# Performance work log

Hardware: AMD Instinct MI355X
Metric: run time of the kernel (lower is better)

## Reference

```python
import jax, jax.numpy as jnp
import numpy as np

NUM_FEATURES = 1_000_000
EMB_DIM = 16
NUM_FIELDS = 39
CIN_SIZES = (200, 200, 200)
DNN_SIZES = (400, 400)


def setup_inputs() -> dict:
    key = jax.random.key(0)
    ks = jax.random.split(key, 16)
    B = 2048
    inp = {}
    inp["feature_ids"] = jax.random.randint(ks[0], (B, NUM_FIELDS), 0, NUM_FEATURES)
    inp["feature_vals"] = jax.random.uniform(ks[1], (B, NUM_FIELDS), dtype=jnp.float32)
    # embeddings (xavier-normal-ish scale)
    inp["emb"] = jax.random.normal(ks[2], (NUM_FEATURES, EMB_DIM), jnp.float32) * 0.02
    inp["bias_emb"] = jax.random.normal(ks[3], (NUM_FEATURES, 1), jnp.float32) * 0.02
    # CIN conv1d (kernel size 1) weights: (out, in)
    field_nums = [NUM_FIELDS]
    for i, size in enumerate(CIN_SIZES):
        cin_in = field_nums[-1] * NUM_FIELDS
        inp[f"cin_W{i}"] = jax.random.normal(ks[4 + i], (size, cin_in), jnp.float32) / np.sqrt(cin_in)
        inp[f"cin_b{i}"] = jnp.zeros((size,), jnp.float32)
        field_nums.append(size // 2 if i != len(CIN_SIZES) - 1 else size)
    # DNN linears: (out, in)
    last = NUM_FIELDS * EMB_DIM
    for i, size in enumerate(DNN_SIZES):
        inp[f"dnn_W{i}"] = jax.random.normal(ks[8 + i], (size, last), jnp.float32) / np.sqrt(last)
        inp[f"dnn_b{i}"] = jnp.zeros((size,), jnp.float32)
        last = size
    hidden_size = sum(CIN_SIZES[:-1]) // 2 + CIN_SIZES[-1]  # 400
    fc_in = hidden_size + DNN_SIZES[-1]
    inp["fc_W"] = jax.random.normal(ks[12], (1, fc_in), jnp.float32) / np.sqrt(fc_in)
    inp["fc_b"] = jnp.zeros((1,), jnp.float32)
    return inp


def _forward(feature_ids, feature_vals, emb, bias_emb,
             cin_W0, cin_b0, cin_W1, cin_b1, cin_W2, cin_b2,
             dnn_W0, dnn_b0, dnn_W1, dnn_b1, fc_W, fc_b):
    B = feature_ids.shape[0]
    inputs = emb[feature_ids] * feature_vals[:, :, None]        # [B, F, D]
    input_biases = bias_emb[feature_ids][..., 0] * feature_vals  # [B, F]

    # CIN
    Ws = (cin_W0, cin_W1, cin_W2)
    bs = (cin_b0, cin_b1, cin_b2)
    h = inputs
    finals = []
    n_layers = len(CIN_SIZES)
    for i in range(n_layers):
        size = CIN_SIZES[i]
        x = jnp.einsum('bhd,bmd->bhmd', h, inputs)              # [B, H, F, D]
        x = x.reshape(B, -1, EMB_DIM)                           # [B, H*F, D]
        x = jnp.einsum('bcd,oc->bod', x, Ws[i]) + bs[i][None, :, None]  # 1x1 conv
        x = jax.nn.relu(x)
        if i != n_layers - 1:
            h, direct = x[:, : size // 2], x[:, size // 2:]
        else:
            direct = x
        finals.append(direct)
    cin_result = jnp.sum(jnp.concatenate(finals, axis=1), axis=-1)  # [B, hidden]

    # DNN
    d = inputs.reshape(B, -1)
    d = jax.nn.relu(d @ dnn_W0.T + dnn_b0)
    d = jax.nn.relu(d @ dnn_W1.T + dnn_b1)

    out = (jnp.concatenate((cin_result, d), axis=1) @ fc_W.T + fc_b)[:, 0]
    return out + jnp.sum(input_biases, axis=1)                  # [B]


def reference(feature_ids, feature_vals, emb, bias_emb,
              cin_W0, cin_b0, cin_W1, cin_b1, cin_W2, cin_b2,
              dnn_W0, dnn_b0, dnn_W1, dnn_b1, fc_W, fc_b):
    return _forward(feature_ids, feature_vals, emb, bias_emb,
                    cin_W0, cin_b0, cin_W1, cin_b1, cin_W2, cin_b2,
                    dnn_W0, dnn_b0, dnn_W1, dnn_b1, fc_W, fc_b)
```

## Files before the change

kernel.cpp:

```cpp
#include <hip/hip_runtime.h>

#define B 2048
#define NF 39
#define D 16

typedef __bf16 bf16x8 __attribute__((ext_vector_type(8)));
typedef float f32x4 __attribute__((ext_vector_type(4)));

__device__ __forceinline__ void lds_barrier() {
  asm volatile("s_waitcnt lgkmcnt(0)" ::: "memory");
  __builtin_amdgcn_s_barrier();
}

__global__ __launch_bounds__(256) void gather_kernel(
    const int* __restrict__ fid, const float* __restrict__ fval,
    const float* __restrict__ emb, const float* __restrict__ bias_emb,
    float* __restrict__ inputs, float* __restrict__ biassum) {
  int b = blockIdx.x;
  __shared__ int ids[NF];
  __shared__ float vals[NF];
  int t = threadIdx.x;
  if (t < NF) { ids[t] = fid[b * NF + t]; vals[t] = fval[b * NF + t]; }
  __syncthreads();
  for (int i = t; i < NF * D; i += 256) {
    int f = i >> 4, d = i & 15;
    inputs[b * NF * D + i] = emb[(long)ids[f] * D + d] * vals[f];
  }
  if (t < 64) {
    float pb = (t < NF) ? bias_emb[ids[t]] * vals[t] : 0.f;
#pragma unroll
    for (int m = 32; m >= 1; m >>= 1) pb += __shfl_xor(pb, m);
    if (t == 0) biassum[b] = pb;
  }
}

__device__ __forceinline__ void prep_cin_one(const float* __restrict__ W,
                                             __bf16* __restrict__ Wg,
                                             int Hreal, int idx) {
  int l = idx & 63;
  int mt = (idx >> 6) % 13;
  int c = idx / (13 * 64);
  int o = mt * 16 + (l & 15);
  int kb = c * 32 + ((l >> 4) << 3);
  int rowlen = Hreal * 39;
  bf16x8 v;
#pragma unroll
  for (int j = 0; j < 8; ++j) {
    int k = kb + j;
    int h = k / 40;
    int m = k - h * 40;
    float val = 0.f;
    if (o < 200 && h < Hreal && m < 39) val = W[(long)o * rowlen + h * 39 + m];
    v[j] = (__bf16)val;
  }
  *reinterpret_cast<bf16x8*>(Wg + (long)idx * 8) = v;
}

__device__ __forceinline__ void prep_dnn_one(const float* __restrict__ W,
                                             __bf16* __restrict__ Wd,
                                             int IN, int idx) {
  int l = idx & 63;
  int tt = (idx >> 6) % 25;
  int c = idx / (25 * 64);
  int o = tt * 16 + (l & 15);
  int kb = c * 32 + ((l >> 4) << 3);
  bf16x8 v;
#pragma unroll
  for (int j = 0; j < 8; ++j) {
    int k = kb + j;
    v[j] = (k < IN) ? (__bf16)W[(long)o * IN + k] : (__bf16)0.f;
  }
  *reinterpret_cast<bf16x8*>(Wd + (long)idx * 8) = v;
}

#define PREP_T0 (50 * 13 * 64)
#define PREP_T12 (126 * 13 * 64)
#define PREP_T3 (20 * 25 * 64)
#define PREP_T4 (13 * 25 * 64)
#define PREP_TOTAL (PREP_T0 + 2 * PREP_T12 + PREP_T3 + PREP_T4)

__global__ void prep_all(const float* __restrict__ cW0, const float* __restrict__ cW1,
                         const float* __restrict__ cW2, const float* __restrict__ dW0,
                         const float* __restrict__ dW1, __bf16* __restrict__ Wg0,
                         __bf16* __restrict__ Wg1, __bf16* __restrict__ Wg2,
                         __bf16* __restrict__ Wd0, __bf16* __restrict__ Wd1) {
  int idx = blockIdx.x * 256 + threadIdx.x;
  if (idx < PREP_T0) { prep_cin_one(cW0, Wg0, 39, idx); return; }
  idx -= PREP_T0;
  if (idx < PREP_T12) { prep_cin_one(cW1, Wg1, 100, idx); return; }
  idx -= PREP_T12;
  if (idx < PREP_T12) { prep_cin_one(cW2, Wg2, 100, idx); return; }
  idx -= PREP_T12;
  if (idx < PREP_T3) { prep_dnn_one(dW0, Wd0, 624, idx); return; }
  idx -= PREP_T3;
  if (idx < PREP_T4) prep_dnn_one(dW1, Wd1, 400, idx);
}

__device__ __forceinline__ void form_x2(const float* Hs, const float* Zs,
                                        __bf16* xbuf, int k0, int col) {
  int h = (int)((unsigned)k0 / 40u);
  int m0 = k0 - h * 40;
  float hv = Hs[h * 32 + col];
  const float4* zp = reinterpret_cast<const float4*>(Zs + col * 44 + m0);
  float4 za = zp[0], zb = zp[1];
  bf16x8 xv;
  xv[0] = (__bf16)(hv * za.x); xv[1] = (__bf16)(hv * za.y);
  xv[2] = (__bf16)(hv * za.z); xv[3] = (__bf16)(hv * za.w);
  xv[4] = (__bf16)(hv * zb.x); xv[5] = (__bf16)(hv * zb.y);
  xv[6] = (__bf16)(hv * zb.z); xv[7] = (__bf16)(hv * zb.w);
  int g = (k0 >> 3) & 7;
  *reinterpret_cast<bf16x8*>(
      reinterpret_cast<char*>(xbuf) + col * 128 + ((g * 16) ^ ((col & 7) << 4))) = xv;
}

template <int PLO, int NP, int NST, int SPLIT>
__device__ __forceinline__ void cin_layer2(
    float* Hs, const float* Zs, __bf16* Xs,
    const __bf16* __restrict__ Wg, const float* __restrict__ bias,
    float* __restrict__ cin_out, int col_offset, int bbase, int t) {
  constexpr int TLO = PLO >> 1;
  constexpr int THI = (PLO + NP - 1) >> 1;
  constexpr int TN = THI - TLO + 1;
  const int l = t & 63;
  const int q = l >> 4, dd = l & 15;
  const int xcol = t & 31;
  const int xg = (t >> 5) & 7;
  const __bf16* wl = Wg + l * 8;

  f32x4 acc[NP] = {};
  bf16x8 wf[TN][2], wfn[TN][2];
#pragma unroll
  for (int i = 0; i < TN; ++i)
#pragma unroll
    for (int c2 = 0; c2 < 2; ++c2)
      wf[i][c2] = *reinterpret_cast<const bf16x8*>(
          wl + (long)((c2 * 13 + TLO + i) * 64) * 8);

  form_x2(Hs, Zs, Xs, xg * 8, xcol);
  lds_barrier();

  for (int s = 0; s < NST; ++s) {
    __bf16* xcur = Xs + (s & 1) * 2048;
    __bf16* xnxt = Xs + ((s + 1) & 1) * 2048;
    const bool more = (s + 1 < NST);
    if (more) {
#pragma unroll
      for (int i = 0; i < TN; ++i)
#pragma unroll
        for (int c2 = 0; c2 < 2; ++c2)
          wfn[i][c2] = *reinterpret_cast<const bf16x8*>(
              wl + (long)((((s + 1) * 2 + c2) * 13 + TLO + i) * 64) * 8);
    }
    bf16x8 bfr[2][2];
#pragma unroll
    for (int f = 0; f < 2; ++f)
#pragma unroll
      for (int c2 = 0; c2 < 2; ++c2) {
        int col = f * 16 + dd;
        int g = c2 * 4 + q;
        bfr[f][c2] = *reinterpret_cast<const bf16x8*>(
            reinterpret_cast<const char*>(xcur) + col * 128 +
            ((g * 16) ^ ((col & 7) << 4)));
      }
    if (more) form_x2(Hs, Zs, xnxt, (s + 1) * 64 + xg * 8, xcol);
    __builtin_amdgcn_s_setprio(1);
#pragma unroll
    for (int i = 0; i < NP; ++i) {
      const int p = PLO + i;
      const int ti = (p >> 1) - TLO;
      const int f = p & 1;
      acc[i] = __builtin_amdgcn_mfma_f32_16x16x32_bf16(wf[ti][0], bfr[f][0],
                                                       acc[i], 0, 0, 0);
      acc[i] = __builtin_amdgcn_mfma_f32_16x16x32_bf16(wf[ti][1], bfr[f][1],
                                                       acc[i], 0, 0, 0);
    }
    __builtin_amdgcn_s_setprio(0);
    lds_barrier();
    if (more) {
#pragma unroll
      for (int i = 0; i < TN; ++i) {
        wf[i][0] = wfn[i][0];
        wf[i][1] = wfn[i][1];
      }
    }
  }

#pragma unroll
  for (int i = 0; i < NP; ++i) {
    const int p = PLO + i;
    const int tt = p >> 1, f = p & 1;
    const int b = bbase + f;
#pragma unroll
    for (int r = 0; r < 4; ++r) {
      int o = tt * 16 + q * 4 + r;
      if (o < 200) {
        float x = fmaxf(acc[i][r] + bias[o], 0.f);
        if (SPLIT && o < 100) {
          Hs[o * 32 + f * 16 + dd] = x;
        } else {
          x += __shfl_xor(x, 1);
          x += __shfl_xor(x, 2);
          x += __shfl_xor(x, 4);
          x += __shfl_xor(x, 8);
          if (dd == 0) cin_out[b * 400 + col_offset + o - (SPLIT ? 100 : 0)] = x;
        }
      }
    }
  }
  lds_barrier();
}

template <int PLO, int NP>
__device__ __forceinline__ void cin_all2(
    float* Hs, const float* Zs, __bf16* Xs, const __bf16* Wg0,
    const __bf16* Wg1, const __bf16* Wg2, const float* cb0, const float* cb1,
    const float* cb2, float* cinres, int bbase, int t) {
  cin_layer2<PLO, NP, 25, 1>(Hs, Zs, Xs, Wg0, cb0, cinres, 0, bbase, t);
  cin_layer2<PLO, NP, 63, 1>(Hs, Zs, Xs, Wg1, cb1, cinres, 100, bbase, t);
  cin_layer2<PLO, NP, 63, 0>(Hs, Zs, Xs, Wg2, cb2, cinres, 200, bbase, t);
}

__global__ __launch_bounds__(256, 4) void cin_fused2(
    const float* __restrict__ Zin, const __bf16* __restrict__ Wg0,
    const __bf16* __restrict__ Wg1, const __bf16* __restrict__ Wg2,
    const float* __restrict__ cb0, const float* __restrict__ cb1,
    const float* __restrict__ cb2, float* __restrict__ cinres) {
  __shared__ float Hs[101 * 32];
  __shared__ float Zs[32 * 44];
  __shared__ __bf16 Xs[2 * 2048];
  const int t = threadIdx.x;
  const int bbase = blockIdx.x * 2;

  for (int i = t; i < 32 * 44; i += 256) {
    int col = i / 44, m = i - (i / 44) * 44;
    int b = bbase + (col >> 4), d = col & 15;
    Zs[i] = (m < NF) ? Zin[((long)b * NF + m) * 16 + d] : 0.f;
  }
  for (int i = t; i < 41 * 32; i += 256) {
    int h = i >> 5, col = i & 31;
    int b = bbase + (col >> 4), d = col & 15;
    Hs[i] = (h < NF) ? Zin[((long)b * NF + h) * 16 + d] : 0.f;
  }
  if (t < 32) Hs[100 * 32 + t] = 0.f;
  __syncthreads();

  const int w = t >> 6;
  switch (w) {
    case 0: cin_all2<0, 7>(Hs, Zs, Xs, Wg0, Wg1, Wg2, cb0, cb1, cb2, cinres, bbase, t); break;
    case 1: cin_all2<7, 7>(Hs, Zs, Xs, Wg0, Wg1, Wg2, cb0, cb1, cb2, cinres, bbase, t); break;
    case 2: cin_all2<14, 6>(Hs, Zs, Xs, Wg0, Wg1, Wg2, cb0, cb1, cb2, cinres, bbase, t); break;
    default: cin_all2<20, 6>(Hs, Zs, Xs, Wg0, Wg1, Wg2, cb0, cb1, cb2, cinres, bbase, t); break;
  }
}

template <int IN>
__device__ __forceinline__ void dnn_stage_load(const float* __restrict__ x,
                                               int bg, int c, int t,
                                               float4& a, float4& b2) {
  int b = t >> 2, kb = t & 3;
  int k0 = c * 32 + kb * 8;
  if (k0 < IN) {
    const float4* p =
        reinterpret_cast<const float4*>(x + (long)(bg * 64 + b) * IN + k0);
    a = p[0];
    b2 = p[1];
  } else {
    a = make_float4(0.f, 0.f, 0.f, 0.f);
    b2 = make_float4(0.f, 0.f, 0.f, 0.f);
  }
}

__device__ __forceinline__ void dnn_stage_write(__bf16* Xs, int t, float4 a,
                                                float4 b2) {
  int b = t >> 2, kb = t & 3;
  bf16x8 v;
  v[0] = (__bf16)a.x;  v[1] = (__bf16)a.y;  v[2] = (__bf16)a.z;  v[3] = (__bf16)a.w;
  v[4] = (__bf16)b2.x; v[5] = (__bf16)b2.y; v[6] = (__bf16)b2.z; v[7] = (__bf16)b2.w;
  *reinterpret_cast<bf16x8*>(Xs + ((kb * 64 + b) << 3)) = v;
}

template <int IN, int NCH>
__global__ __launch_bounds__(256) void dnn_mfma2(
    const float* __restrict__ x, const __bf16* __restrict__ Wd,
    const float* __restrict__ bias, float* __restrict__ out) {
  __shared__ __bf16 Xs[2 * 2048];
  const int bg = blockIdx.x / 25;
  const int tile = blockIdx.x - bg * 25;
  const int t = threadIdx.x;
  const int w = t >> 6, l = t & 63;
  const int q = l >> 4, dd = l & 15;
  const __bf16* wl = Wd + l * 8;

  f32x4 acc = {};
  bf16x8 wf = *reinterpret_cast<const bf16x8*>(wl + (long)(tile * 64) * 8);

  float4 ra, rb;
  dnn_stage_load<IN>(x, bg, 0, t, ra, rb);
  dnn_stage_write(Xs, t, ra, rb);
  lds_barrier();

  for (int c = 0; c < NCH; ++c) {
    __bf16* cur = Xs + (c & 1) * 2048;
    __bf16* nxt = Xs + ((c + 1) & 1) * 2048;
    const bool more = (c + 1 < NCH);
    bf16x8 wfn;
    if (more) {
      dnn_stage_load<IN>(x, bg, c + 1, t, ra, rb);
      wfn = *reinterpret_cast<const bf16x8*>(
          wl + (long)(((c + 1) * 25 + tile) * 64) * 8);
    }
    bf16x8 bfr = *reinterpret_cast<const bf16x8*>(cur + ((q * 64 + w * 16 + dd) << 3));
    acc = __builtin_amdgcn_mfma_f32_16x16x32_bf16(wf, bfr, acc, 0, 0, 0);
    if (more) dnn_stage_write(nxt, t, ra, rb);
    lds_barrier();
    if (more) wf = wfn;
  }

  const int b = bg * 64 + w * 16 + dd;
#pragma unroll
  for (int r = 0; r < 4; ++r) {
    int o = tile * 16 + q * 4 + r;
    out[(long)b * 400 + o] = fmaxf(acc[r] + bias[o], 0.f);
  }
}

__global__ __launch_bounds__(256) void final_kernel(
    const float* __restrict__ cin, const float* __restrict__ d1,
    const float* __restrict__ fcW, const float* __restrict__ fcb,
    const float* __restrict__ biassum, float* __restrict__ out) {
  int b = blockIdx.x, t = threadIdx.x;
  float p = 0.f;
  for (int i = t; i < 800; i += 256) {
    float v = (i < 400) ? cin[b * 400 + i] : d1[b * 400 + (i - 400)];
    p += v * fcW[i];
  }
#pragma unroll
  for (int m = 32; m >= 1; m >>= 1) p += __shfl_xor(p, m);
  __shared__ float red[4];
  if ((t & 63) == 0) red[t >> 6] = p;
  __syncthreads();
  if (t == 0) out[b] = red[0] + red[1] + red[2] + red[3] + fcb[0] + biassum[b];
}

extern "C" void kernel_launch(void* const* d_in, const int* in_sizes, int n_in,
                              void* d_out, int out_size, void* d_ws,
                              size_t ws_size, hipStream_t stream) {
  (void)in_sizes; (void)n_in; (void)out_size; (void)ws_size;
  const int* fid = (const int*)d_in[0];
  const float* fval = (const float*)d_in[1];
  const float* emb = (const float*)d_in[2];
  const float* bias_emb = (const float*)d_in[3];
  const float* cW0 = (const float*)d_in[4];
  const float* cb0 = (const float*)d_in[5];
  const float* cW1 = (const float*)d_in[6];
  const float* cb1 = (const float*)d_in[7];
  const float* cW2 = (const float*)d_in[8];
  const float* cb2 = (const float*)d_in[9];
  const float* dW0 = (const float*)d_in[10];
  const float* db0 = (const float*)d_in[11];
  const float* dW1 = (const float*)d_in[12];
  const float* db1 = (const float*)d_in[13];
  const float* fcW = (const float*)d_in[14];
  const float* fcb = (const float*)d_in[15];
  float* out = (float*)d_out;

  float* ws = (float*)d_ws;
  float* inputs = ws;  ws += B * NF * D;
  float* biassum = ws; ws += B;
  float* cinres = ws;  ws += B * 400;
  float* dd0 = ws;     ws += B * 400;
  float* dd1 = ws;     ws += B * 400;
  __bf16* Wg0 = (__bf16*)ws; ws += (50 * 13 * 64 * 8) / 2;
  __bf16* Wg1 = (__bf16*)ws; ws += (126 * 13 * 64 * 8) / 2;
  __bf16* Wg2 = (__bf16*)ws; ws += (126 * 13 * 64 * 8) / 2;
  __bf16* Wd0 = (__bf16*)ws; ws += (20 * 25 * 64 * 8) / 2;
  __bf16* Wd1 = (__bf16*)ws; ws += (13 * 25 * 64 * 8) / 2;

  gather_kernel<<<B, 256, 0, stream>>>(fid, fval, emb, bias_emb, inputs, biassum);

  prep_all<<<(PREP_TOTAL + 255) / 256, 256, 0, stream>>>(
      cW0, cW1, cW2, dW0, dW1, Wg0, Wg1, Wg2, Wd0, Wd1);

  cin_fused2<<<B / 2, 256, 0, stream>>>(inputs, Wg0, Wg1, Wg2, cb0, cb1, cb2, cinres);

  dnn_mfma2<624, 20><<<32 * 25, 256, 0, stream>>>(inputs, Wd0, db0, dd0);
  dnn_mfma2<400, 13><<<32 * 25, 256, 0, stream>>>(dd0, Wd1, db1, dd1);

  final_kernel<<<B, 256, 0, stream>>>(cinres, dd1, fcW, fcb, biassum, out);
}
```

Baseline: 234.5 us.

## Process four batch rows per CIN block with 2D wave tiling and ping-pong weight registers

```diff
diff --git a/kernel.cpp b/kernel.cpp
--- a/kernel.cpp
+++ b/kernel.cpp
@@ -96,11 +96,11 @@
   if (idx < PREP_T4) prep_dnn_one(dW1, Wd1, 400, idx);
 }
 
-__device__ __forceinline__ void form_x2(const float* Hs, const float* Zs,
-                                        __bf16* xbuf, int k0, int col) {
+__device__ __forceinline__ void form_x(const float* Hs, const float* Zs,
+                                       __bf16* xbuf, int k0, int col) {
   int h = (int)((unsigned)k0 / 40u);
   int m0 = k0 - h * 40;
-  float hv = Hs[h * 32 + col];
+  float hv = Hs[h * 64 + col];
   const float4* zp = reinterpret_cast<const float4*>(Zs + col * 44 + m0);
   float4 za = zp[0], zb = zp[1];
   bf16x8 xv;
@@ -113,96 +113,98 @@
       reinterpret_cast<char*>(xbuf) + col * 128 + ((g * 16) ^ ((col & 7) << 4))) = xv;
 }
 
-template <int PLO, int NP, int NST, int SPLIT>
-__device__ __forceinline__ void cin_layer2(
+template <int TLO, int TN, int FLO, bool PRE>
+__device__ __forceinline__ void cin_stage(
+    bf16x8 (&wf_use)[TN * 2], bf16x8 (&wf_load)[TN * 2], f32x4 (&acc)[TN * 2],
+    float* Hs, const float* Zs, __bf16* Xs, const __bf16* wl,
+    int s, int q, int dd, int xg, int l) {
+  __bf16* xcur = Xs + (s & 1) * 4096;
+  if (PRE) {
+#pragma unroll
+    for (int i = 0; i < TN; ++i)
+#pragma unroll
+      for (int cc = 0; cc < 2; ++cc)
+        wf_load[i * 2 + cc] = *reinterpret_cast<const bf16x8*>(
+            wl + (long)((((s + 1) * 2 + cc) * 13 + TLO + i) * 64) * 8);
+  }
+  bf16x8 bfr[2][2];
+#pragma unroll
+  for (int f2 = 0; f2 < 2; ++f2)
+#pragma unroll
+    for (int cc = 0; cc < 2; ++cc) {
+      int col = (FLO + f2) * 16 + dd;
+      int g = cc * 4 + q;
+      bfr[f2][cc] = *reinterpret_cast<const bf16x8*>(
+          reinterpret_cast<const char*>(xcur) + col * 128 +
+          ((g * 16) ^ ((col & 7) << 4)));
+    }
+  if (PRE) {
+    __bf16* xnxt = Xs + ((s + 1) & 1) * 4096;
+    form_x(Hs, Zs, xnxt, (s + 1) * 64 + xg * 8, l);
+    form_x(Hs, Zs, xnxt, (s + 1) * 64 + (xg + 4) * 8, l);
+  }
+  __builtin_amdgcn_s_setprio(1);
+#pragma unroll
+  for (int i = 0; i < TN; ++i)
+#pragma unroll
+    for (int f2 = 0; f2 < 2; ++f2)
+#pragma unroll
+      for (int cc = 0; cc < 2; ++cc)
+        acc[i * 2 + f2] = __builtin_amdgcn_mfma_f32_16x16x32_bf16(
+            wf_use[i * 2 + cc], bfr[f2][cc], acc[i * 2 + f2], 0, 0, 0);
+  __builtin_amdgcn_s_setprio(0);
+  lds_barrier();
+}
+
+template <int TLO, int TN, int FLO, int NST, int SPLIT>
+__device__ __forceinline__ void cin_layer3(
     float* Hs, const float* Zs, __bf16* Xs,
     const __bf16* __restrict__ Wg, const float* __restrict__ bias,
     float* __restrict__ cin_out, int col_offset, int bbase, int t) {
-  constexpr int TLO = PLO >> 1;
-  constexpr int THI = (PLO + NP - 1) >> 1;
-  constexpr int TN = THI - TLO + 1;
   const int l = t & 63;
   const int q = l >> 4, dd = l & 15;
-  const int xcol = t & 31;
-  const int xg = (t >> 5) & 7;
+  const int xg = t >> 6;
   const __bf16* wl = Wg + l * 8;
 
-  f32x4 acc[NP] = {};
-  bf16x8 wf[TN][2], wfn[TN][2];
+  f32x4 acc[TN * 2] = {};
+  bf16x8 wfA[TN * 2], wfB[TN * 2];
 #pragma unroll
   for (int i = 0; i < TN; ++i)
 #pragma unroll
-    for (int c2 = 0; c2 < 2; ++c2)
-      wf[i][c2] = *reinterpret_cast<const bf16x8*>(
-          wl + (long)((c2 * 13 + TLO + i) * 64) * 8);
-
-  form_x2(Hs, Zs, Xs, xg * 8, xcol);
+    for (int cc = 0; cc < 2; ++cc)
+      wfA[i * 2 + cc] = *reinterpret_cast<const bf16x8*>(
+          wl + (long)((cc * 13 + TLO + i) * 64) * 8);
+  form_x(Hs, Zs, Xs, xg * 8, l);
+  form_x(Hs, Zs, Xs, (xg + 4) * 8, l);
   lds_barrier();
 
-  for (int s = 0; s < NST; ++s) {
-    __bf16* xcur = Xs + (s & 1) * 2048;
-    __bf16* xnxt = Xs + ((s + 1) & 1) * 2048;
-    const bool more = (s + 1 < NST);
-    if (more) {
-#pragma unroll
-      for (int i = 0; i < TN; ++i)
-#pragma unroll
-        for (int c2 = 0; c2 < 2; ++c2)
-          wfn[i][c2] = *reinterpret_cast<const bf16x8*>(
-              wl + (long)((((s + 1) * 2 + c2) * 13 + TLO + i) * 64) * 8);
-    }
-    bf16x8 bfr[2][2];
-#pragma unroll
-    for (int f = 0; f < 2; ++f)
-#pragma unroll
-      for (int c2 = 0; c2 < 2; ++c2) {
-        int col = f * 16 + dd;
-        int g = c2 * 4 + q;
-        bfr[f][c2] = *reinterpret_cast<const bf16x8*>(
-            reinterpret_cast<const char*>(xcur) + col * 128 +
-            ((g * 16) ^ ((col & 7) << 4)));
-      }
-    if (more) form_x2(Hs, Zs, xnxt, (s + 1) * 64 + xg * 8, xcol);
-    __builtin_amdgcn_s_setprio(1);
-#pragma unroll
-    for (int i = 0; i < NP; ++i) {
-      const int p = PLO + i;
-      const int ti = (p >> 1) - TLO;
-      const int f = p & 1;
-      acc[i] = __builtin_amdgcn_mfma_f32_16x16x32_bf16(wf[ti][0], bfr[f][0],
-                                                       acc[i], 0, 0, 0);
-      acc[i] = __builtin_amdgcn_mfma_f32_16x16x32_bf16(wf[ti][1], bfr[f][1],
-                                                       acc[i], 0, 0, 0);
-    }
-    __builtin_amdgcn_s_setprio(0);
-    lds_barrier();
-    if (more) {
-#pragma unroll
-      for (int i = 0; i < TN; ++i) {
-        wf[i][0] = wfn[i][0];
-        wf[i][1] = wfn[i][1];
-      }
-    }
-  }
-
-#pragma unroll
-  for (int i = 0; i < NP; ++i) {
-    const int p = PLO + i;
-    const int tt = p >> 1, f = p & 1;
-    const int b = bbase + f;
-#pragma unroll
-    for (int r = 0; r < 4; ++r) {
-      int o = tt * 16 + q * 4 + r;
-      if (o < 200) {
-        float x = fmaxf(acc[i][r] + bias[o], 0.f);
-        if (SPLIT && o < 100) {
-          Hs[o * 32 + f * 16 + dd] = x;
-        } else {
-          x += __shfl_xor(x, 1);
-          x += __shfl_xor(x, 2);
-          x += __shfl_xor(x, 4);
-          x += __shfl_xor(x, 8);
-          if (dd == 0) cin_out[b * 400 + col_offset + o - (SPLIT ? 100 : 0)] = x;
+  for (int s2 = 0; s2 < (NST - 1) / 2; ++s2) {
+    cin_stage<TLO, TN, FLO, true>(wfA, wfB, acc, Hs, Zs, Xs, wl, 2 * s2, q, dd, xg, l);
+    cin_stage<TLO, TN, FLO, true>(wfB, wfA, acc, Hs, Zs, Xs, wl, 2 * s2 + 1, q, dd, xg, l);
+  }
+  cin_stage<TLO, TN, FLO, false>(wfA, wfB, acc, Hs, Zs, Xs, wl, NST - 1, q, dd, xg, l);
+
+#pragma unroll
+  for (int i = 0; i < TN; ++i) {
+    const int tt = TLO + i;
+#pragma unroll
+    for (int f2 = 0; f2 < 2; ++f2) {
+      const int f = FLO + f2;
+      const int b = bbase + f;
+#pragma unroll
+      for (int r = 0; r < 4; ++r) {
+        int o = tt * 16 + q * 4 + r;
+        if (o < 200) {
+          float x = fmaxf(acc[i * 2 + f2][r] + bias[o], 0.f);
+          if (SPLIT && o < 100) {
+            Hs[o * 64 + f * 16 + dd] = x;
+          } else {
+            x += __shfl_xor(x, 1);
+            x += __shfl_xor(x, 2);
+            x += __shfl_xor(x, 4);
+            x += __shfl_xor(x, 8);
+            if (dd == 0) cin_out[b * 400 + col_offset + o - (SPLIT ? 100 : 0)] = x;
+          }
         }
       }
     }
@@ -210,46 +212,46 @@
   lds_barrier();
 }
 
-template <int PLO, int NP>
-__device__ __forceinline__ void cin_all2(
+template <int TLO, int TN, int FLO>
+__device__ __forceinline__ void cin_all3(
     float* Hs, const float* Zs, __bf16* Xs, const __bf16* Wg0,
     const __bf16* Wg1, const __bf16* Wg2, const float* cb0, const float* cb1,
     const float* cb2, float* cinres, int bbase, int t) {
-  cin_layer2<PLO, NP, 25, 1>(Hs, Zs, Xs, Wg0, cb0, cinres, 0, bbase, t);
-  cin_layer2<PLO, NP, 63, 1>(Hs, Zs, Xs, Wg1, cb1, cinres, 100, bbase, t);
-  cin_layer2<PLO, NP, 63, 0>(Hs, Zs, Xs, Wg2, cb2, cinres, 200, bbase, t);
-}
-
-__global__ __launch_bounds__(256, 4) void cin_fused2(
+  cin_layer3<TLO, TN, FLO, 25, 1>(Hs, Zs, Xs, Wg0, cb0, cinres, 0, bbase, t);
+  cin_layer3<TLO, TN, FLO, 63, 1>(Hs, Zs, Xs, Wg1, cb1, cinres, 100, bbase, t);
+  cin_layer3<TLO, TN, FLO, 63, 0>(Hs, Zs, Xs, Wg2, cb2, cinres, 200, bbase, t);
+}
+
+__global__ __launch_bounds__(256, 2) void cin_fused3(
     const float* __restrict__ Zin, const __bf16* __restrict__ Wg0,
     const __bf16* __restrict__ Wg1, const __bf16* __restrict__ Wg2,
     const float* __restrict__ cb0, const float* __restrict__ cb1,
     const float* __restrict__ cb2, float* __restrict__ cinres) {
-  __shared__ float Hs[101 * 32];
-  __shared__ float Zs[32 * 44];
-  __shared__ __bf16 Xs[2 * 2048];
+  __shared__ float Hs[101 * 64];
+  __shared__ float Zs[64 * 44];
+  __shared__ __bf16 Xs[2 * 64 * 64];
   const int t = threadIdx.x;
-  const int bbase = blockIdx.x * 2;
-
-  for (int i = t; i < 32 * 44; i += 256) {
+  const int bbase = blockIdx.x * 4;
+
+  for (int i = t; i < 64 * 44; i += 256) {
     int col = i / 44, m = i - (i / 44) * 44;
     int b = bbase + (col >> 4), d = col & 15;
     Zs[i] = (m < NF) ? Zin[((long)b * NF + m) * 16 + d] : 0.f;
   }
-  for (int i = t; i < 41 * 32; i += 256) {
-    int h = i >> 5, col = i & 31;
+  for (int i = t; i < 41 * 64; i += 256) {
+    int h = i >> 6, col = i & 63;
     int b = bbase + (col >> 4), d = col & 15;
     Hs[i] = (h < NF) ? Zin[((long)b * NF + h) * 16 + d] : 0.f;
   }
-  if (t < 32) Hs[100 * 32 + t] = 0.f;
+  if (t < 64) Hs[100 * 64 + t] = 0.f;
   __syncthreads();
 
   const int w = t >> 6;
   switch (w) {
-    case 0: cin_all2<0, 7>(Hs, Zs, Xs, Wg0, Wg1, Wg2, cb0, cb1, cb2, cinres, bbase, t); break;
-    case 1: cin_all2<7, 7>(Hs, Zs, Xs, Wg0, Wg1, Wg2, cb0, cb1, cb2, cinres, bbase, t); break;
-    case 2: cin_all2<14, 6>(Hs, Zs, Xs, Wg0, Wg1, Wg2, cb0, cb1, cb2, cinres, bbase, t); break;
-    default: cin_all2<20, 6>(Hs, Zs, Xs, Wg0, Wg1, Wg2, cb0, cb1, cb2, cinres, bbase, t); break;
+    case 0: cin_all3<0, 7, 0>(Hs, Zs, Xs, Wg0, Wg1, Wg2, cb0, cb1, cb2, cinres, bbase, t); break;
+    case 1: cin_all3<0, 7, 2>(Hs, Zs, Xs, Wg0, Wg1, Wg2, cb0, cb1, cb2, cinres, bbase, t); break;
+    case 2: cin_all3<7, 6, 0>(Hs, Zs, Xs, Wg0, Wg1, Wg2, cb0, cb1, cb2, cinres, bbase, t); break;
+    default: cin_all3<7, 6, 2>(Hs, Zs, Xs, Wg0, Wg1, Wg2, cb0, cb1, cb2, cinres, bbase, t); break;
   }
 }
 
@@ -381,7 +383,7 @@
   prep_all<<<(PREP_TOTAL + 255) / 256, 256, 0, stream>>>(
       cW0, cW1, cW2, dW0, dW1, Wg0, Wg1, Wg2, Wd0, Wd1);
 
-  cin_fused2<<<B / 2, 256, 0, stream>>>(inputs, Wg0, Wg1, Wg2, cb0, cb1, cb2, cinres);
+  cin_fused3<<<B / 4, 256, 0, stream>>>(inputs, Wg0, Wg1, Wg2, cb0, cb1, cb2, cinres);
 
   dnn_mfma2<624, 20><<<32 * 25, 256, 0, stream>>>(inputs, Wd0, db0, dd0);
   dnn_mfma2<400, 13><<<32 * 25, 256, 0, stream>>>(dd0, Wd1, db1, dd1);
```

Result: faster. 204.8 us (-12.6%).

## Process four batch rows per CIN block and store H/Z tiles as bf16

Applied to the files above, without the earlier changes.

```diff
diff --git a/kernel.cpp b/kernel.cpp
--- a/kernel.cpp
+++ b/kernel.cpp
@@ -96,99 +96,91 @@
   if (idx < PREP_T4) prep_dnn_one(dW1, Wd1, 400, idx);
 }
 
-__device__ __forceinline__ void form_x2(const float* Hs, const float* Zs,
-                                        __bf16* xbuf, int k0, int col) {
+__device__ __forceinline__ void form_x(const __bf16* Hs, const __bf16* Zs,
+                                       __bf16* xbuf, int k0, int col) {
   int h = (int)((unsigned)k0 / 40u);
   int m0 = k0 - h * 40;
-  float hv = Hs[h * 32 + col];
-  const float4* zp = reinterpret_cast<const float4*>(Zs + col * 44 + m0);
-  float4 za = zp[0], zb = zp[1];
+  float hv = (float)Hs[h * 64 + col];
+  bf16x8 z = *reinterpret_cast<const bf16x8*>(Zs + col * 40 + m0);
   bf16x8 xv;
-  xv[0] = (__bf16)(hv * za.x); xv[1] = (__bf16)(hv * za.y);
-  xv[2] = (__bf16)(hv * za.z); xv[3] = (__bf16)(hv * za.w);
-  xv[4] = (__bf16)(hv * zb.x); xv[5] = (__bf16)(hv * zb.y);
-  xv[6] = (__bf16)(hv * zb.z); xv[7] = (__bf16)(hv * zb.w);
+#pragma unroll
+  for (int j = 0; j < 8; ++j) xv[j] = (__bf16)(hv * (float)z[j]);
   int g = (k0 >> 3) & 7;
-  *reinterpret_cast<bf16x8*>(
-      reinterpret_cast<char*>(xbuf) + col * 128 + ((g * 16) ^ ((col & 7) << 4))) = xv;
-}
-
-template <int PLO, int NP, int NST, int SPLIT>
-__device__ __forceinline__ void cin_layer2(
-    float* Hs, const float* Zs, __bf16* Xs,
+  *reinterpret_cast<bf16x8*>(reinterpret_cast<char*>(xbuf) + g * 1024 + col * 16) = xv;
+}
+
+template <int W, int NST, int SPLIT>
+__device__ __forceinline__ void cin_layer(
+    __bf16* Hs, const __bf16* Zs, __bf16* Xs,
     const __bf16* __restrict__ Wg, const float* __restrict__ bias,
     float* __restrict__ cin_out, int col_offset, int bbase, int t) {
-  constexpr int TLO = PLO >> 1;
-  constexpr int THI = (PLO + NP - 1) >> 1;
-  constexpr int TN = THI - TLO + 1;
+  constexpr int TLO = (13 * W) >> 2;
   const int l = t & 63;
   const int q = l >> 4, dd = l & 15;
-  const int xcol = t & 31;
-  const int xg = (t >> 5) & 7;
-  const __bf16* wl = Wg + l * 8;
-
-  f32x4 acc[NP] = {};
-  bf16x8 wf[TN][2], wfn[TN][2];
-#pragma unroll
-  for (int i = 0; i < TN; ++i)
-#pragma unroll
-    for (int c2 = 0; c2 < 2; ++c2)
-      wf[i][c2] = *reinterpret_cast<const bf16x8*>(
-          wl + (long)((c2 * 13 + TLO + i) * 64) * 8);
-
-  form_x2(Hs, Zs, Xs, xg * 8, xcol);
+
+  f32x4 acc[13] = {};
+  bf16x8 wf[8], wfn[8];
+  const __bf16* wp = Wg + l * 8 + TLO * 512;
+#pragma unroll
+  for (int i = 0; i < 4; ++i)
+#pragma unroll
+    for (int hf = 0; hf < 2; ++hf)
+      wf[i * 2 + hf] = *reinterpret_cast<const bf16x8*>(wp + hf * 6656 + i * 512);
+
+  form_x(Hs, Zs, Xs, W * 8, l);
+  form_x(Hs, Zs, Xs, (W + 4) * 8, l);
   lds_barrier();
 
   for (int s = 0; s < NST; ++s) {
-    __bf16* xcur = Xs + (s & 1) * 2048;
-    __bf16* xnxt = Xs + ((s + 1) & 1) * 2048;
+    __bf16* xcur = Xs + (s & 1) * 4096;
+    __bf16* xnxt = Xs + ((s + 1) & 1) * 4096;
     const bool more = (s + 1 < NST);
     if (more) {
-#pragma unroll
-      for (int i = 0; i < TN; ++i)
-#pragma unroll
-        for (int c2 = 0; c2 < 2; ++c2)
-          wfn[i][c2] = *reinterpret_cast<const bf16x8*>(
-              wl + (long)((((s + 1) * 2 + c2) * 13 + TLO + i) * 64) * 8);
-    }
-    bf16x8 bfr[2][2];
-#pragma unroll
-    for (int f = 0; f < 2; ++f)
-#pragma unroll
-      for (int c2 = 0; c2 < 2; ++c2) {
-        int col = f * 16 + dd;
-        int g = c2 * 4 + q;
-        bfr[f][c2] = *reinterpret_cast<const bf16x8*>(
-            reinterpret_cast<const char*>(xcur) + col * 128 +
-            ((g * 16) ^ ((col & 7) << 4)));
+      const __bf16* wq = wp + 13312;
+#pragma unroll
+      for (int i = 0; i < 4; ++i)
+#pragma unroll
+        for (int hf = 0; hf < 2; ++hf)
+          wfn[i * 2 + hf] =
+              *reinterpret_cast<const bf16x8*>(wq + hf * 6656 + i * 512);
+    }
+    bf16x8 bfr[4][2];
+#pragma unroll
+    for (int f = 0; f < 4; ++f)
+#pragma unroll
+      for (int hf = 0; hf < 2; ++hf) {
+        bfr[f][hf] = *reinterpret_cast<const bf16x8*>(
+            reinterpret_cast<const char*>(xcur) + (hf * 4 + q) * 1024 +
+            (f * 16 + dd) * 16);
       }
-    if (more) form_x2(Hs, Zs, xnxt, (s + 1) * 64 + xg * 8, xcol);
+    if (more) {
+      form_x(Hs, Zs, xnxt, (s + 1) * 64 + W * 8, l);
+      form_x(Hs, Zs, xnxt, (s + 1) * 64 + (W + 4) * 8, l);
+    }
     __builtin_amdgcn_s_setprio(1);
 #pragma unroll
-    for (int i = 0; i < NP; ++i) {
-      const int p = PLO + i;
-      const int ti = (p >> 1) - TLO;
-      const int f = p & 1;
-      acc[i] = __builtin_amdgcn_mfma_f32_16x16x32_bf16(wf[ti][0], bfr[f][0],
+    for (int i = 0; i < 13; ++i) {
+      const int p = 13 * W + i;
+      const int ti = (p >> 2) - TLO;
+      const int f = p & 3;
+      acc[i] = __builtin_amdgcn_mfma_f32_16x16x32_bf16(wf[ti * 2 + 0], bfr[f][0],
                                                        acc[i], 0, 0, 0);
-      acc[i] = __builtin_amdgcn_mfma_f32_16x16x32_bf16(wf[ti][1], bfr[f][1],
+      acc[i] = __builtin_amdgcn_mfma_f32_16x16x32_bf16(wf[ti * 2 + 1], bfr[f][1],
                                                        acc[i], 0, 0, 0);
     }
     __builtin_amdgcn_s_setprio(0);
     lds_barrier();
     if (more) {
 #pragma unroll
-      for (int i = 0; i < TN; ++i) {
-        wf[i][0] = wfn[i][0];
-        wf[i][1] = wfn[i][1];
-      }
-    }
-  }
-
-#pragma unroll
-  for (int i = 0; i < NP; ++i) {
-    const int p = PLO + i;
-    const int tt = p >> 1, f = p & 1;
+      for (int i = 0; i < 8; ++i) wf[i] = wfn[i];
+      wp += 13312;
+    }
+  }
+
+#pragma unroll
+  for (int i = 0; i < 13; ++i) {
+    const int p = 13 * W + i;
+    const int tt = p >> 2, f = p & 3;
     const int b = bbase + f;
 #pragma unroll
     for (int r = 0; r < 4; ++r) {
@@ -196,7 +188,7 @@
       if (o < 200) {
         float x = fmaxf(acc[i][r] + bias[o], 0.f);
         if (SPLIT && o < 100) {
-          Hs[o * 32 + f * 16 + dd] = x;
+          Hs[o * 64 + f * 16 + dd] = (__bf16)x;
         } else {
           x += __shfl_xor(x, 1);
           x += __shfl_xor(x, 2);
@@ -210,46 +202,46 @@
   lds_barrier();
 }
 
-template <int PLO, int NP>
-__device__ __forceinline__ void cin_all2(
-    float* Hs, const float* Zs, __bf16* Xs, const __bf16* Wg0,
+template <int W>
+__device__ __forceinline__ void cin_all(
+    __bf16* Hs, const __bf16* Zs, __bf16* Xs, const __bf16* Wg0,
     const __bf16* Wg1, const __bf16* Wg2, const float* cb0, const float* cb1,
     const float* cb2, float* cinres, int bbase, int t) {
-  cin_layer2<PLO, NP, 25, 1>(Hs, Zs, Xs, Wg0, cb0, cinres, 0, bbase, t);
-  cin_layer2<PLO, NP, 63, 1>(Hs, Zs, Xs, Wg1, cb1, cinres, 100, bbase, t);
-  cin_layer2<PLO, NP, 63, 0>(Hs, Zs, Xs, Wg2, cb2, cinres, 200, bbase, t);
-}
-
-__global__ __launch_bounds__(256, 4) void cin_fused2(
+  cin_layer<W, 25, 1>(Hs, Zs, Xs, Wg0, cb0, cinres, 0, bbase, t);
+  cin_layer<W, 63, 1>(Hs, Zs, Xs, Wg1, cb1, cinres, 100, bbase, t);
+  cin_layer<W, 63, 0>(Hs, Zs, Xs, Wg2, cb2, cinres, 200, bbase, t);
+}
+
+__global__ __launch_bounds__(256, 4) void cin_fused4(
     const float* __restrict__ Zin, const __bf16* __restrict__ Wg0,
     const __bf16* __restrict__ Wg1, const __bf16* __restrict__ Wg2,
     const float* __restrict__ cb0, const float* __restrict__ cb1,
     const float* __restrict__ cb2, float* __restrict__ cinres) {
-  __shared__ float Hs[101 * 32];
-  __shared__ float Zs[32 * 44];
-  __shared__ __bf16 Xs[2 * 2048];
+  __shared__ __bf16 Hs[101 * 64];
+  __shared__ __bf16 Zs[64 * 40];
+  __shared__ __bf16 Xs[2 * 4096];
   const int t = threadIdx.x;
-  const int bbase = blockIdx.x * 2;
-
-  for (int i = t; i < 32 * 44; i += 256) {
-    int col = i / 44, m = i - (i / 44) * 44;
+  const int bbase = blockIdx.x * 4;
+
+  for (int i = t; i < 64 * 40; i += 256) {
+    int col = i / 40, m = i - (i / 40) * 40;
     int b = bbase + (col >> 4), d = col & 15;
-    Zs[i] = (m < NF) ? Zin[((long)b * NF + m) * 16 + d] : 0.f;
-  }
-  for (int i = t; i < 41 * 32; i += 256) {
-    int h = i >> 5, col = i & 31;
+    Zs[i] = (m < NF) ? (__bf16)Zin[((long)b * NF + m) * 16 + d] : (__bf16)0.f;
+  }
+  for (int i = t; i < 41 * 64; i += 256) {
+    int h = i >> 6, col = i & 63;
     int b = bbase + (col >> 4), d = col & 15;
-    Hs[i] = (h < NF) ? Zin[((long)b * NF + h) * 16 + d] : 0.f;
-  }
-  if (t < 32) Hs[100 * 32 + t] = 0.f;
+    Hs[i] = (h < NF) ? (__bf16)Zin[((long)b * NF + h) * 16 + d] : (__bf16)0.f;
+  }
+  if (t < 64) Hs[100 * 64 + t] = (__bf16)0.f;
   __syncthreads();
 
   const int w = t >> 6;
   switch (w) {
-    case 0: cin_all2<0, 7>(Hs, Zs, Xs, Wg0, Wg1, Wg2, cb0, cb1, cb2, cinres, bbase, t); break;
-    case 1: cin_all2<7, 7>(Hs, Zs, Xs, Wg0, Wg1, Wg2, cb0, cb1, cb2, cinres, bbase, t); break;
-    case 2: cin_all2<14, 6>(Hs, Zs, Xs, Wg0, Wg1, Wg2, cb0, cb1, cb2, cinres, bbase, t); break;
-    default: cin_all2<20, 6>(Hs, Zs, Xs, Wg0, Wg1, Wg2, cb0, cb1, cb2, cinres, bbase, t); break;
+    case 0: cin_all<0>(Hs, Zs, Xs, Wg0, Wg1, Wg2, cb0, cb1, cb2, cinres, bbase, t); break;
+    case 1: cin_all<1>(Hs, Zs, Xs, Wg0, Wg1, Wg2, cb0, cb1, cb2, cinres, bbase, t); break;
+    case 2: cin_all<2>(Hs, Zs, Xs, Wg0, Wg1, Wg2, cb0, cb1, cb2, cinres, bbase, t); break;
+    default: cin_all<3>(Hs, Zs, Xs, Wg0, Wg1, Wg2, cb0, cb1, cb2, cinres, bbase, t); break;
   }
 }
 
@@ -381,7 +373,7 @@
   prep_all<<<(PREP_TOTAL + 255) / 256, 256, 0, stream>>>(
       cW0, cW1, cW2, dW0, dW1, Wg0, Wg1, Wg2, Wd0, Wd1);
 
-  cin_fused2<<<B / 2, 256, 0, stream>>>(inputs, Wg0, Wg1, Wg2, cb0, cb1, cb2, cinres);
+  cin_fused4<<<B / 4, 256, 0, stream>>>(inputs, Wg0, Wg1, Wg2, cb0, cb1, cb2, cinres);
 
   dnn_mfma2<624, 20><<<32 * 25, 256, 0, stream>>>(inputs, Wd0, db0, dd0);
   dnn_mfma2<400, 13><<<32 * 25, 256, 0, stream>>>(dd0, Wd1, db1, dd1);
```

Measured after the change: 746.6 us. 3.18x slower.
